# Performance work log

Measured on AMD Instinct MI355X. Metric: run time of the kernel, lower is better.

The kernel has to match this reference:

```python
import jax, jax.numpy as jnp
import numpy as np

A = 14      # num abnormalities (hardcoded 14 W_Q Linears)
QD = 64     # query_dim
H = 12      # num_heads
CH = 768    # cls_hidden_dim == H * QD (required by residual add)
B = 4096    # batch


def _layernorm(x, g, b, eps=1e-5):
    m = jnp.mean(x, axis=-1, keepdims=True)
    v = jnp.mean((x - m) ** 2, axis=-1, keepdims=True)
    return (x - m) * jax.lax.rsqrt(v + eps) * g + b


def setup_inputs() -> dict:
    key = jax.random.key(0)
    ks = jax.random.split(key, 9)
    s = 0.02
    return dict(
        classification_queries=jax.random.normal(ks[0], (A, QD), dtype=jnp.float32),
        cls_token=jax.random.normal(ks[1], (B, A, CH), dtype=jnp.float32),
        WQ=jax.random.normal(ks[2], (A, QD, QD), dtype=jnp.float32) * s,  # 14 per-abnormality query projections
        bQ=jnp.zeros((A, QD), dtype=jnp.float32),
        WK=jax.random.normal(ks[3], (H, CH, QD), dtype=jnp.float32) * s,  # per-head K projections
        bK=jnp.zeros((H, QD), dtype=jnp.float32),
        WV=jax.random.normal(ks[4], (H, CH, QD), dtype=jnp.float32) * s,  # per-head V projections
        bV=jnp.zeros((H, QD), dtype=jnp.float32),
        W1=jax.random.normal(ks[5], (H * QD, CH), dtype=jnp.float32) * s,
        b1=jnp.zeros((CH,), dtype=jnp.float32),
        W2=jax.random.normal(ks[6], (CH, CH), dtype=jnp.float32) * s,
        b2=jnp.zeros((CH,), dtype=jnp.float32),
        g1=jnp.ones((CH,), dtype=jnp.float32),
        be1=jnp.zeros((CH,), dtype=jnp.float32),
        g2=jnp.ones((CH,), dtype=jnp.float32),
        be2=jnp.zeros((CH,), dtype=jnp.float32),
    )


def reference(classification_queries, cls_token, WQ, bQ, WK, bK, WV, bV,
              W1, b1, W2, b2, g1, be1, g2, be2):
    dt = cls_token.dtype
    scale = jnp.asarray(float(QD) ** 0.5, dt)
    # Per-abnormality query projection (batched over the 14 Linears): [A, QD]
    Q = jnp.einsum('ad,adq->aq', classification_queries, WQ) + bQ
    # Per-head K/V projections, batched over heads: [B, H, S, QD] with S == A == 14
    K = jnp.einsum('bsc,hcq->bhsq', cls_token, WK) + bK[None, :, None, :]
    V = jnp.einsum('bsc,hcq->bhsq', cls_token, WV) + bV[None, :, None, :]
    # Attention scores: [B, H, A, S]; Q is broadcast across batch (torch expand)
    scores = jnp.einsum('aq,bhsq->bhas', Q, K) / scale
    # NOTE: original applies softmax over dim=1 of [B, A, S] -> the query axis 'a'
    attn = jax.nn.softmax(scores, axis=2)
    # Weighted values, heads concatenated on last dim: [B, A, H*QD]
    out = jnp.einsum('bhas,bhsq->bahq', attn, V).reshape(cls_token.shape[0], A, H * QD)
    x = _layernorm(cls_token + out, g1, be1)
    ff = jnp.maximum(jnp.dot(x, W1) + b1, 0.0) @ W2 + b2
    return _layernorm(x + ff, g2, be2)
```

## Files before the change

kernel.cpp:

```cpp
#include <hip/hip_runtime.h>
#include <stdint.h>

#define B_  4096
#define A_  14
#define QD_ 64
#define H_  12
#define CH_ 768
#define M_  (B_*A_)
#define NS_ (H_*A_)
#define N1_ (CH_+NS_)

typedef float  f32x4  __attribute__((ext_vector_type(4)));
typedef short  bf16x8 __attribute__((ext_vector_type(8)));
typedef short  s16x4  __attribute__((ext_vector_type(4)));
typedef int    i32x4  __attribute__((ext_vector_type(4)));

__device__ __forceinline__ float b2f(ushort u) {
  union { uint32_t u; float f; } c; c.u = ((uint32_t)u) << 16; return c.f;
}
__device__ __forceinline__ ushort f2b(float f) {
  union { float f; uint32_t u; } c; c.f = f;
  uint32_t u = c.u;
  return (ushort)((u + 0x7FFFu + ((u >> 16) & 1u)) >> 16);
}


__global__ void prep_q(const float* __restrict__ cq, const float* __restrict__ WQ,
                       const float* __restrict__ bQ, float* __restrict__ Qout) {
  for (int i = threadIdx.x; i < A_*QD_; i += 256) {
    int a = i >> 6, q = i & 63;
    float acc = bQ[i];
    for (int d = 0; d < 64; ++d) acc += cq[a*64 + d] * WQ[(a*64 + d)*64 + q];
    Qout[i] = acc;
  }
}

__global__ void prep_wcat(const float* __restrict__ WV, const float* __restrict__ bV,
                          const float* __restrict__ WK, const float* __restrict__ bK,
                          const float* __restrict__ Qb, ushort* __restrict__ Wcat,
                          float* __restrict__ biascat) {
  int n = blockIdx.x, t = threadIdx.x;
  if (n < CH_) {
    int h = n >> 6, q = n & 63;
    for (int c = t; c < CH_; c += 256)
      Wcat[(size_t)n*CH_ + c] = f2b(WV[((size_t)h*CH_ + c)*64 + q]);
    if (t == 0) biascat[n] = bV[n];
  } else if (n < N1_) {
    int j = n - CH_; int h = j / 14, a = j % 14;
    __shared__ float qrow[64];
    if (t < 64) qrow[t] = Qb[a*64 + t];
    __syncthreads();
    for (int c = t; c < CH_; c += 256) {
      const float* wk = WK + ((size_t)h*CH_ + c)*64;
      float acc = 0.f;
      #pragma unroll
      for (int q = 0; q < 64; ++q) acc += qrow[q] * wk[q];
      Wcat[(size_t)n*CH_ + c] = f2b(acc * 0.125f);
    }
    if (t == 0) {
      float acc = 0.f;
      for (int q = 0; q < 64; ++q) acc += qrow[q] * bK[h*64 + q];
      biascat[n] = acc * 0.125f;
    }
  } else {
    for (int c = t; c < CH_; c += 256) Wcat[(size_t)n*CH_ + c] = 0;
    if (t == 0) biascat[n] = 0.f;
  }
}

__global__ void prep_wt(const float* __restrict__ W1, const float* __restrict__ W2,
                        ushort* __restrict__ W1T, ushort* __restrict__ W2T) {
  int i = blockIdx.x;
  int n = (i < CH_) ? i : i - CH_;
  const float* W = (i < CH_) ? W1 : W2;
  ushort* O = (i < CH_) ? W1T : W2T;
  for (int k = threadIdx.x; k < CH_; k += 256)
    O[(size_t)n*CH_ + k] = f2b(W[(size_t)k*CH_ + n]);
}

__global__ void prep_cls(const float* __restrict__ cls, ushort* __restrict__ out) {
  const size_t n4 = (size_t)M_*CH_/4;
  for (size_t i = (size_t)blockIdx.x*256 + threadIdx.x; i < n4; i += (size_t)gridDim.x*256) {
    const float* p = cls + i*4;
    s16x4 o;
    o[0] = (short)f2b(p[0]); o[1] = (short)f2b(p[1]);
    o[2] = (short)f2b(p[2]); o[3] = (short)f2b(p[3]);
    *(s16x4*)(out + i*4) = o;
  }
}

template<int MODE>
__global__ __launch_bounds__(256)
void gemm_k(const ushort* __restrict__ Ap, const ushort* __restrict__ Bp,
            const float* __restrict__ bias,
            ushort* __restrict__ Cb, float* __restrict__ Sout) {
  const int tid = threadIdx.x;
  const int wave = tid >> 6, lane = tid & 63;
  const int wm = wave >> 1, wn = wave & 1;
  const int m0 = blockIdx.y * 128, n0 = blockIdx.x * 128;

  __shared__ __align__(16) ushort Asm[128*64];
  __shared__ __align__(16) ushort Bsm[128*64];

  f32x4 acc[4][4] = {};

  const int srow0  = wave*32 + (lane >> 3);
  const int schunk = lane & 7;

  for (int kt = 0; kt < 12; ++kt) {
    const int k0 = kt * 64;
    #pragma unroll
    for (int i = 0; i < 4; ++i) {
      const int row = srow0 + i*8;
      const int dby = row*128 + ((schunk ^ (row & 7)) * 16);
      i32x4 av = *(const i32x4*)(Ap + (size_t)(m0 + row)*CH_ + k0 + schunk*8);
      i32x4 bv = *(const i32x4*)(Bp + (size_t)(n0 + row)*CH_ + k0 + schunk*8);
      *(i32x4*)((char*)Asm + dby) = av;
      *(i32x4*)((char*)Bsm + dby) = bv;
    }
    __syncthreads();
    #pragma unroll
    for (int kk = 0; kk < 2; ++kk) {
      bf16x8 af[4], bfr[4];
      #pragma unroll
      for (int f = 0; f < 4; ++f) {
        int ar = wm*64 + f*16 + (lane & 15);
        int ab = ar*128 + kk*64 + (lane >> 4)*16;
        ab ^= (ar & 7) << 4;
        af[f] = *(const bf16x8*)((const char*)Asm + ab);
        int br = wn*64 + f*16 + (lane & 15);
        int bb = br*128 + kk*64 + (lane >> 4)*16;
        bb ^= (br & 7) << 4;
        bfr[f] = *(const bf16x8*)((const char*)Bsm + bb);
      }
      #pragma unroll
      for (int i = 0; i < 4; ++i)
        #pragma unroll
        for (int j = 0; j < 4; ++j)
          acc[i][j] = __builtin_amdgcn_mfma_f32_16x16x32_bf16(af[i], bfr[j], acc[i][j], 0, 0, 0);
    }
    __syncthreads();
  }

  #pragma unroll
  for (int j = 0; j < 4; ++j) {
    const int gc = n0 + wn*64 + j*16 + (lane & 15);
    const float bv = bias[gc];
    #pragma unroll
    for (int i = 0; i < 4; ++i) {
      const int gr0 = m0 + wm*64 + i*16 + ((lane >> 4) << 2);
      #pragma unroll
      for (int r = 0; r < 4; ++r) {
        const float v = acc[i][j][r] + bv;
        const int gr = gr0 + r;
        if (MODE == 0) {
          if (gc < CH_) {
            Cb[(size_t)gr*CH_ + gc] = f2b(v);
          } else if (gc < N1_) {
            const int j2 = gc - CH_;
            const int h = j2 / 14, a = j2 % 14;
            const int b = gr / 14, s = gr % 14;
            Sout[(((size_t)b*H_ + h)*A_ + a)*A_ + s] = v;
          }
        } else if (MODE == 1) {
          Cb[(size_t)gr*CH_ + gc] = f2b(fmaxf(v, 0.f));
        } else {
          Cb[(size_t)gr*CH_ + gc] = f2b(v);
        }
      }
    }
  }
}

__global__ __launch_bounds__(256)
void attn_ln1(const float* __restrict__ Sbuf, const ushort* __restrict__ Vbuf,
              const float* __restrict__ cls, const float* __restrict__ g1,
              const float* __restrict__ be1, ushort* __restrict__ xout) {
  const int b = blockIdx.x, tid = threadIdx.x;
  const int wave = tid >> 6, lane = tid & 63;
  __shared__ __align__(16) float  s_sc[H_*A_*A_];
  __shared__ __align__(16) ushort s_v[A_*CH_];
  __shared__ __align__(16) float  s_out[A_*CH_];

  for (int i = tid; i < H_*A_*A_; i += 256) s_sc[i] = Sbuf[(size_t)b*H_*A_*A_ + i];
  for (int i = tid; i < A_*CH_/8; i += 256)
    *(i32x4*)((char*)s_v + i*16) = *(const i32x4*)((const char*)(Vbuf + (size_t)b*A_*CH_) + i*16);
  __syncthreads();

  if (tid < H_*A_) {
    int h = tid / 14, s = tid % 14;
    float vals[14], mx = -1e30f;
    #pragma unroll
    for (int a = 0; a < 14; ++a) { float v = s_sc[(h*14 + a)*14 + s]; vals[a] = v; mx = fmaxf(mx, v); }
    float sum = 0.f;
    #pragma unroll
    for (int a = 0; a < 14; ++a) { float e = __expf(vals[a] - mx); vals[a] = e; sum += e; }
    float inv = 1.f / sum;
    #pragma unroll
    for (int a = 0; a < 14; ++a) s_sc[(h*14 + a)*14 + s] = vals[a] * inv;
  }
  __syncthreads();

  for (int idx = tid; idx < A_*(CH_/4); idx += 256) {
    int a = idx / (CH_/4), c = (idx % (CH_/4)) * 4;
    int h = c >> 6;
    const float* at = &s_sc[(h*14 + a)*14];
    float a0 = 0.f, a1 = 0.f, a2 = 0.f, a3 = 0.f;
    #pragma unroll
    for (int s = 0; s < 14; ++s) {
      float w = at[s];
      s16x4 vv = *(const s16x4*)(&s_v[s*CH_ + c]);
      a0 += w * b2f((ushort)vv[0]); a1 += w * b2f((ushort)vv[1]);
      a2 += w * b2f((ushort)vv[2]); a3 += w * b2f((ushort)vv[3]);
    }
    f32x4 st; st[0] = a0; st[1] = a1; st[2] = a2; st[3] = a3;
    *(f32x4*)(&s_out[a*CH_ + c]) = st;
  }
  __syncthreads();

  for (int a = wave; a < A_; a += 4) {
    const f32x4* crow = (const f32x4*)(cls + ((size_t)b*A_ + a)*CH_);
    f32x4 vr[3]; float sum = 0.f, sq = 0.f;
    #pragma unroll
    for (int j = 0; j < 3; ++j) {
      f32x4 cv = crow[lane + j*64];
      f32x4 ov = *(const f32x4*)(&s_out[a*CH_ + (lane + j*64)*4]);
      f32x4 t = cv + ov;
      vr[j] = t;
      #pragma unroll
      for (int u = 0; u < 4; ++u) { sum += t[u]; sq += t[u]*t[u]; }
    }
    #pragma unroll
    for (int off = 32; off >= 1; off >>= 1) {
      sum += __shfl_xor(sum, off, 64);
      sq  += __shfl_xor(sq,  off, 64);
    }
    float mean = sum * (1.f/768.f);
    float var  = sq * (1.f/768.f) - mean*mean;
    float rstd = rsqrtf(var + 1e-5f);
    #pragma unroll
    for (int j = 0; j < 3; ++j) {
      int c = (lane + j*64)*4;
      f32x4 gv = *(const f32x4*)(g1 + c);
      f32x4 bv = *(const f32x4*)(be1 + c);
      s16x4 pk;
      #pragma unroll
      for (int u = 0; u < 4; ++u)
        pk[u] = (short)f2b((vr[j][u] - mean)*rstd*gv[u] + bv[u]);
      *(s16x4*)(&xout[((size_t)b*A_ + a)*CH_ + c]) = pk;
    }
  }
}

__global__ __launch_bounds__(256)
void ln2_k(const ushort* __restrict__ xb, const ushort* __restrict__ yb,
           const float* __restrict__ g2, const float* __restrict__ be2,
           float* __restrict__ out) {
  const int row = blockIdx.x*4 + (threadIdx.x >> 6);
  const int lane = threadIdx.x & 63;
  const ushort* xr = xb + (size_t)row*CH_;
  const ushort* yr = yb + (size_t)row*CH_;
  float v[12]; float sum = 0.f, sq = 0.f;
  #pragma unroll
  for (int j = 0; j < 3; ++j) {
    int c = (lane + j*64)*4;
    s16x4 xv = *(const s16x4*)(xr + c);
    s16x4 yv = *(const s16x4*)(yr + c);
    #pragma unroll
    for (int u = 0; u < 4; ++u) {
      float t = b2f((ushort)xv[u]) + b2f((ushort)yv[u]);
      v[j*4 + u] = t; sum += t; sq += t*t;
    }
  }
  #pragma unroll
  for (int off = 32; off >= 1; off >>= 1) {
    sum += __shfl_xor(sum, off, 64);
    sq  += __shfl_xor(sq,  off, 64);
  }
  float mean = sum * (1.f/768.f);
  float var  = sq * (1.f/768.f) - mean*mean;
  float rstd = rsqrtf(var + 1e-5f);
  float* orow = out + (size_t)row*CH_;
  #pragma unroll
  for (int j = 0; j < 3; ++j) {
    int c = (lane + j*64)*4;
    f32x4 gv = *(const f32x4*)(g2 + c);
    f32x4 bv = *(const f32x4*)(be2 + c);
    f32x4 o;
    #pragma unroll
    for (int u = 0; u < 4; ++u) o[u] = (v[j*4+u] - mean)*rstd*gv[u] + bv[u];
    *(f32x4*)(orow + c) = o;
  }
}

extern "C" void kernel_launch(void* const* d_in, const int* in_sizes, int n_in,
                              void* d_out, int out_size, void* d_ws, size_t ws_size,
                              hipStream_t stream) {
  const float* cq  = (const float*)d_in[0];
  const float* cls = (const float*)d_in[1];
  const float* WQ  = (const float*)d_in[2];
  const float* bQ  = (const float*)d_in[3];
  const float* WK  = (const float*)d_in[4];
  const float* bK  = (const float*)d_in[5];
  const float* WV  = (const float*)d_in[6];
  const float* bV  = (const float*)d_in[7];
  const float* W1  = (const float*)d_in[8];
  const float* b1  = (const float*)d_in[9];
  const float* W2  = (const float*)d_in[10];
  const float* b2  = (const float*)d_in[11];
  const float* g1  = (const float*)d_in[12];
  const float* be1 = (const float*)d_in[13];
  const float* g2  = (const float*)d_in[14];
  const float* be2 = (const float*)d_in[15];
  float* out = (float*)d_out;

  char* ws = (char*)d_ws;
  float*  qbuf    = (float*)(ws + 0);
  float*  biascat = (float*)(ws + 4096);
  ushort* wcat    = (ushort*)(ws + 8192);
  ushort* w1t     = (ushort*)(ws + 1581056);
  ushort* w2t     = (ushort*)(ws + 2760704);
  ushort* clsbf   = (ushort*)(ws + 4194304);
  ushort* vbuf    = (ushort*)(ws + 92274688);
  float*  sbuf    = (float*)(ws + 180355072);
  ushort* ybuf    = (ushort*)(ws + 218890240);
  ushort* xbuf  = clsbf;
  ushort* h1buf = vbuf;

  prep_q   <<<1,    256, 0, stream>>>(cq, WQ, bQ, qbuf);
  prep_wcat<<<1024, 256, 0, stream>>>(WV, bV, WK, bK, qbuf, wcat, biascat);
  prep_wt  <<<1536, 256, 0, stream>>>(W1, W2, w1t, w2t);
  prep_cls <<<2048, 256, 0, stream>>>(cls, clsbf);

  gemm_k<0><<<dim3(8, 448), 256, 0, stream>>>(clsbf, wcat, biascat, vbuf, sbuf);
  attn_ln1 <<<B_, 256, 0, stream>>>(sbuf, vbuf, cls, g1, be1, xbuf);
  gemm_k<1><<<dim3(6, 448), 256, 0, stream>>>(xbuf, w1t, b1, h1buf, nullptr);
  gemm_k<2><<<dim3(6, 448), 256, 0, stream>>>(h1buf, w2t, b2, ybuf, nullptr);
  ln2_k    <<<M_/4, 256, 0, stream>>>(xbuf, ybuf, g2, be2, out);
}
```

Baseline: 727.1 us.

## Use direct global-to-LDS loads, XCD-aware tile remap, and fuse attention output into LN1

The GEMM tile loads now go straight from global memory into LDS through global_load_lds 16-byte transfers, with the XOR swizzle folded into the source address, so the data no longer passes through registers. Block IDs are remapped so that consecutive tiles land on the same XCD, which should improve L2 reuse of the shared operand tiles. In attn_ln1 the attention-weighted V sum is computed inline inside the layernorm loop, removing the s_out shared buffer, one barrier and the LDS round trip. This lowers LDS usage and may raise occupancy, but the direct-to-LDS path relies on the specific lane-to-address layout being correct.

```diff
diff --git a/kernel.cpp b/kernel.cpp
--- a/kernel.cpp
+++ b/kernel.cpp
@@ -14,6 +14,10 @@
 typedef short  bf16x8 __attribute__((ext_vector_type(8)));
 typedef short  s16x4  __attribute__((ext_vector_type(4)));
 typedef int    i32x4  __attribute__((ext_vector_type(4)));
+
+#define GLOAD_LDS16(gp, lp) \
+  __builtin_amdgcn_global_load_lds((const __attribute__((address_space(1))) void*)(gp), \
+                                   (__attribute__((address_space(3))) void*)(lp), 16, 0, 0)
 
 __device__ __forceinline__ float b2f(ushort u) {
   union { uint32_t u; float f; } c; c.u = ((uint32_t)u) << 16; return c.f;
@@ -94,29 +98,33 @@
 void gemm_k(const ushort* __restrict__ Ap, const ushort* __restrict__ Bp,
             const float* __restrict__ bias,
             ushort* __restrict__ Cb, float* __restrict__ Sout) {
+  constexpr int GX = (MODE == 0) ? 8 : 6;
+  constexpr int NWG = GX * 448;
   const int tid = threadIdx.x;
   const int wave = tid >> 6, lane = tid & 63;
   const int wm = wave >> 1, wn = wave & 1;
-  const int m0 = blockIdx.y * 128, n0 = blockIdx.x * 128;
+
+  const int bid = blockIdx.x;
+  const int tl = (bid & 7) * (NWG >> 3) + (bid >> 3);
+  const int m0 = (tl / GX) * 128, n0 = (tl % GX) * 128;
 
   __shared__ __align__(16) ushort Asm[128*64];
   __shared__ __align__(16) ushort Bsm[128*64];
 
   f32x4 acc[4][4] = {};
 
-  const int srow0  = wave*32 + (lane >> 3);
-  const int schunk = lane & 7;
+  const int rc = lane >> 3;
+  const int sc = (lane & 7) ^ rc;
+  const ushort* Abase = Ap + (size_t)(m0 + rc)*CH_ + sc*8;
+  const ushort* Bbase = Bp + (size_t)(n0 + rc)*CH_ + sc*8;
 
   for (int kt = 0; kt < 12; ++kt) {
     const int k0 = kt * 64;
     #pragma unroll
-    for (int i = 0; i < 4; ++i) {
-      const int row = srow0 + i*8;
-      const int dby = row*128 + ((schunk ^ (row & 7)) * 16);
-      i32x4 av = *(const i32x4*)(Ap + (size_t)(m0 + row)*CH_ + k0 + schunk*8);
-      i32x4 bv = *(const i32x4*)(Bp + (size_t)(n0 + row)*CH_ + k0 + schunk*8);
-      *(i32x4*)((char*)Asm + dby) = av;
-      *(i32x4*)((char*)Bsm + dby) = bv;
+    for (int ci = 0; ci < 4; ++ci) {
+      const int c = wave*4 + ci;
+      GLOAD_LDS16(Abase + (size_t)c*8*CH_ + k0, &Asm[c*512]);
+      GLOAD_LDS16(Bbase + (size_t)c*8*CH_ + k0, &Bsm[c*512]);
     }
     __syncthreads();
     #pragma unroll
@@ -125,12 +133,10 @@
       #pragma unroll
       for (int f = 0; f < 4; ++f) {
         int ar = wm*64 + f*16 + (lane & 15);
-        int ab = ar*128 + kk*64 + (lane >> 4)*16;
-        ab ^= (ar & 7) << 4;
+        int ab = (ar*128 + kk*64 + (lane >> 4)*16) ^ ((ar & 7) << 4);
         af[f] = *(const bf16x8*)((const char*)Asm + ab);
         int br = wn*64 + f*16 + (lane & 15);
-        int bb = br*128 + kk*64 + (lane >> 4)*16;
-        bb ^= (br & 7) << 4;
+        int bb = (br*128 + kk*64 + (lane >> 4)*16) ^ ((br & 7) << 4);
         bfr[f] = *(const bf16x8*)((const char*)Bsm + bb);
       }
       #pragma unroll
@@ -180,7 +186,6 @@
   const int wave = tid >> 6, lane = tid & 63;
   __shared__ __align__(16) float  s_sc[H_*A_*A_];
   __shared__ __align__(16) ushort s_v[A_*CH_];
-  __shared__ __align__(16) float  s_out[A_*CH_];
 
   for (int i = tid; i < H_*A_*A_; i += 256) s_sc[i] = Sbuf[(size_t)b*H_*A_*A_ + i];
   for (int i = tid; i < A_*CH_/8; i += 256)
@@ -201,31 +206,23 @@
   }
   __syncthreads();
 
-  for (int idx = tid; idx < A_*(CH_/4); idx += 256) {
-    int a = idx / (CH_/4), c = (idx % (CH_/4)) * 4;
-    int h = c >> 6;
-    const float* at = &s_sc[(h*14 + a)*14];
-    float a0 = 0.f, a1 = 0.f, a2 = 0.f, a3 = 0.f;
-    #pragma unroll
-    for (int s = 0; s < 14; ++s) {
-      float w = at[s];
-      s16x4 vv = *(const s16x4*)(&s_v[s*CH_ + c]);
-      a0 += w * b2f((ushort)vv[0]); a1 += w * b2f((ushort)vv[1]);
-      a2 += w * b2f((ushort)vv[2]); a3 += w * b2f((ushort)vv[3]);
-    }
-    f32x4 st; st[0] = a0; st[1] = a1; st[2] = a2; st[3] = a3;
-    *(f32x4*)(&s_out[a*CH_ + c]) = st;
-  }
-  __syncthreads();
-
   for (int a = wave; a < A_; a += 4) {
-    const f32x4* crow = (const f32x4*)(cls + ((size_t)b*A_ + a)*CH_);
     f32x4 vr[3]; float sum = 0.f, sq = 0.f;
     #pragma unroll
     for (int j = 0; j < 3; ++j) {
-      f32x4 cv = crow[lane + j*64];
-      f32x4 ov = *(const f32x4*)(&s_out[a*CH_ + (lane + j*64)*4]);
-      f32x4 t = cv + ov;
+      const int c = (lane + j*64) * 4;
+      const int h = c >> 6;
+      const float* at = &s_sc[(h*14 + a)*14];
+      f32x4 acc = {};
+      #pragma unroll
+      for (int s = 0; s < 14; ++s) {
+        float w = at[s];
+        s16x4 vv = *(const s16x4*)(&s_v[s*CH_ + c]);
+        acc[0] += w * b2f((ushort)vv[0]); acc[1] += w * b2f((ushort)vv[1]);
+        acc[2] += w * b2f((ushort)vv[2]); acc[3] += w * b2f((ushort)vv[3]);
+      }
+      f32x4 cv = *(const f32x4*)(cls + ((size_t)b*A_ + a)*CH_ + c);
+      f32x4 t = cv + acc;
       vr[j] = t;
       #pragma unroll
       for (int u = 0; u < 4; ++u) { sum += t[u]; sq += t[u]*t[u]; }
@@ -332,9 +329,9 @@
   prep_wt  <<<1536, 256, 0, stream>>>(W1, W2, w1t, w2t);
   prep_cls <<<2048, 256, 0, stream>>>(cls, clsbf);
 
-  gemm_k<0><<<dim3(8, 448), 256, 0, stream>>>(clsbf, wcat, biascat, vbuf, sbuf);
+  gemm_k<0><<<8*448, 256, 0, stream>>>(clsbf, wcat, biascat, vbuf, sbuf);
   attn_ln1 <<<B_, 256, 0, stream>>>(sbuf, vbuf, cls, g1, be1, xbuf);
-  gemm_k<1><<<dim3(6, 448), 256, 0, stream>>>(xbuf, w1t, b1, h1buf, nullptr);
-  gemm_k<2><<<dim3(6, 448), 256, 0, stream>>>(h1buf, w2t, b2, ybuf, nullptr);
+  gemm_k<1><<<6*448, 256, 0, stream>>>(xbuf, w1t, b1, h1buf, nullptr);
+  gemm_k<2><<<6*448, 256, 0, stream>>>(h1buf, w2t, b2, ybuf, nullptr);
   ln2_k    <<<M_/4, 256, 0, stream>>>(xbuf, ybuf, g2, be2, out);
 }
```

After: 669.8 us. 1.09x faster.
